# Optimization experiments

Hardware: AMD Instinct MI355X
Metric: run time of the kernel (lower is better)

Reference implementation:

```python
import jax, jax.numpy as jnp
import numpy as np

TOPK = 2
NUM_EXPERTS = 8

def setup_inputs() -> dict:
    key = jax.random.key(0)
    kx, kg, k1, k3, k2 = jax.random.split(key, 5)
    B, S, D, F, E = 1, 2048, 1024, 1024, NUM_EXPERTS
    x = jax.random.normal(kx, (B, S, D), dtype=jnp.float32)
    wg = jax.random.normal(kg, (E, D), dtype=jnp.float32) * (1.0 / np.sqrt(D))
    w1 = jax.random.normal(k1, (E, D, F), dtype=jnp.float32) * (1.0 / np.sqrt(D))
    w3 = jax.random.normal(k3, (E, D, F), dtype=jnp.float32) * (1.0 / np.sqrt(D))
    w2 = jax.random.normal(k2, (E, F, D), dtype=jnp.float32) * (1.0 / np.sqrt(F))
    return {"x": x, "wg": wg, "w1": w1, "w3": w3, "w2": w2}

def reference(x, wg, w1, w3, w2):
    # x: [B, S, D] -> tokens [N, D]
    D = x.shape[-1]
    E = wg.shape[0]
    xt = x.reshape(-1, D)
    # Gating: Linear(no bias) + softmax over experts
    logits = xt @ wg.T                      # [N, E]
    gates = jax.nn.softmax(logits, axis=-1)
    # Top-k selection, normalize weights (normalize_expert_weights=True),
    # routed_scaling_factor = 1.0
    weights, idx = jax.lax.top_k(gates, TOPK)      # [N, k]
    weights = weights / weights.sum(axis=-1, keepdims=True)
    # Per-token per-expert combine weight (dispatch+combine equivalent)
    comb = (jax.nn.one_hot(idx, E, dtype=xt.dtype) * weights[..., None]).sum(axis=1)  # [N, E]
    # SwiGLU experts (grouped GEMM equivalent, dense over experts)
    h = jnp.einsum('nd,edf->enf', xt, w1)   # gate proj
    u = jnp.einsum('nd,edf->enf', xt, w3)   # up proj
    a = jax.nn.silu(h) * u                  # [E, N, F]
    out = jnp.einsum('enf,efd,ne->nd', a, w2, comb)
    return out.reshape(x.shape), logits
```

## Files before the change

### kernel.cpp

```cpp
#include <hip/hip_runtime.h>
#include <stdint.h>

typedef unsigned short u16;
typedef __attribute__((ext_vector_type(8))) __bf16 bf16x8;
typedef __attribute__((ext_vector_type(4))) float f32x4;

#define MAXMT 40
#define N_TOK 2048
#define DDIM 1024
#define FDIM 1024

#define DEV static __device__ __forceinline__

DEV float bf2f(u16 u) {
    union { uint32_t i; float f; } v;
    v.i = ((uint32_t)u) << 16;
    return v.f;
}
DEV u16 f2bf(float f) {
    union { float f; uint32_t i; } v;
    v.f = f;
    uint32_t x = v.i;
    return (u16)((x + 0x7fffu + ((x >> 16) & 1u)) >> 16);
}

DEV void async_copy16(const u16* gsrc, u16* ldst) {
    __builtin_amdgcn_global_load_lds(
        (const __attribute__((address_space(1))) void*)(uintptr_t)gsrc,
        (__attribute__((address_space(3))) void*)(uint32_t)(uintptr_t)ldst,
        16, 0, 0);
}

DEV int sniff_fp(const void* p, int tid, int* scnt) {
    if (tid == 0) *scnt = 0;
    __syncthreads();
    u16 u = ((const u16*)p)[tid & 255];
    int e = (u >> 7) & 0xff;
    if (e != 0 && (e < 90 || e > 160)) atomicAdd(scnt, 1);
    __syncthreads();
    return *scnt > 64;
}

__global__ void k_mega(const void* __restrict__ x, const void* __restrict__ wg,
                       const void* __restrict__ w1, const void* __restrict__ w3,
                       const void* __restrict__ w2, u16* __restrict__ wt,
                       u16* __restrict__ xb, void* __restrict__ out_base,
                       int* __restrict__ te, float* __restrict__ tw) {
    __shared__ int scnt;
    __shared__ __align__(16) u16 sT[2][64 * 68];
    int z = blockIdx.z, tid = threadIdx.x;

    if (z >= 2) {
        int zz = z - 2;
        int mat = zz * 2 + (blockIdx.x >> 3);
        int which = mat >> 3, lm = mat & 7;
        const void* src0 = which == 0 ? w1 : (which == 1 ? w3 : w2);
        int fp = sniff_fp(src0, tid, &scnt);
        u16* dst = wt + (size_t)mat * 1048576;
        int rg = tid >> 4, cg = tid & 15;
        int r0 = blockIdx.y * 64, c0 = (blockIdx.x & 7) * 128;
        int rbase = r0 + rg * 4, cbase = c0 + cg * 4;

        u16 vA[4][4], vB[4][4];
        if (fp) {
            const float* sp = (const float*)src0 + (size_t)lm * 1048576;
            float4 fA[4], fB[4];
#pragma unroll
            for (int i = 0; i < 4; i++) fA[i] = *(const float4*)(sp + (size_t)(rbase + i) * 1024 + cbase);
#pragma unroll
            for (int i = 0; i < 4; i++) fB[i] = *(const float4*)(sp + (size_t)(rbase + i) * 1024 + cbase + 64);
#pragma unroll
            for (int i = 0; i < 4; i++) {
                vA[i][0] = f2bf(fA[i].x); vA[i][1] = f2bf(fA[i].y);
                vA[i][2] = f2bf(fA[i].z); vA[i][3] = f2bf(fA[i].w);
                vB[i][0] = f2bf(fB[i].x); vB[i][1] = f2bf(fB[i].y);
                vB[i][2] = f2bf(fB[i].z); vB[i][3] = f2bf(fB[i].w);
            }
        } else {
            const u16* sp = (const u16*)src0 + (size_t)lm * 1048576;
            uint2 uA[4], uB[4];
#pragma unroll
            for (int i = 0; i < 4; i++) uA[i] = *(const uint2*)(sp + (size_t)(rbase + i) * 1024 + cbase);
#pragma unroll
            for (int i = 0; i < 4; i++) uB[i] = *(const uint2*)(sp + (size_t)(rbase + i) * 1024 + cbase + 64);
#pragma unroll
            for (int i = 0; i < 4; i++) { *(uint2*)&vA[i][0] = uA[i]; *(uint2*)&vB[i][0] = uB[i]; }
        }
#pragma unroll
        for (int j = 0; j < 4; j++) {
            uint2 wa, wb;
            wa.x = (uint32_t)vA[0][j] | ((uint32_t)vA[1][j] << 16);
            wa.y = (uint32_t)vA[2][j] | ((uint32_t)vA[3][j] << 16);
            wb.x = (uint32_t)vB[0][j] | ((uint32_t)vB[1][j] << 16);
            wb.y = (uint32_t)vB[2][j] | ((uint32_t)vB[3][j] << 16);
            *(uint2*)&sT[0][(cg * 4 + j) * 68 + rg * 4] = wa;
            *(uint2*)&sT[1][(cg * 4 + j) * 68 + rg * 4] = wb;
        }
        __syncthreads();
        int cc = tid >> 2, seg = tid & 3;
#pragma unroll
        for (int b = 0; b < 2; b++) {
            const u16* spp = &sT[b][cc * 68 + seg * 16];
            uint2 q0 = *(const uint2*)(spp);
            uint2 q1 = *(const uint2*)(spp + 4);
            uint2 q2 = *(const uint2*)(spp + 8);
            uint2 q3 = *(const uint2*)(spp + 12);
            u16* dp = dst + (size_t)(c0 + b * 64 + cc) * 1024 + r0 + seg * 16;
            uint4 o0, o1;
            o0.x = q0.x; o0.y = q0.y; o0.z = q1.x; o0.w = q1.y;
            o1.x = q2.x; o1.y = q2.y; o1.z = q3.x; o1.w = q3.y;
            *(uint4*)dp = o0;
            *(uint4*)(dp + 8) = o1;
        }
    } else {
        int fp = sniff_fp(x, tid, &scnt);
        int gi = z * 256 + blockIdx.y * 16 + blockIdx.x;
        int wave = tid >> 6, lane = tid & 63;
        int n = gi * 4 + wave;
        float acc[8];
#pragma unroll
        for (int e = 0; e < 8; e++) acc[e] = 0.f;
        if (fp) {
            const float* xp = (const float*)x + (size_t)n * DDIM;
            const float* wp = (const float*)wg;
#pragma unroll
            for (int it = 0; it < 4; ++it) {
                int d = it * 256 + lane * 4;
                float4 xv = *(const float4*)(xp + d);
                u16 pk[4] = { f2bf(xv.x), f2bf(xv.y), f2bf(xv.z), f2bf(xv.w) };
                *(uint2*)&xb[(size_t)n * DDIM + d] = *(const uint2*)pk;
#pragma unroll
                for (int e = 0; e < 8; e++) {
                    float4 w4 = *(const float4*)(wp + e * DDIM + d);
                    acc[e] += xv.x * w4.x + xv.y * w4.y + xv.z * w4.z + xv.w * w4.w;
                }
            }
        } else {
            const u16* xp = (const u16*)x + (size_t)n * DDIM;
            const u16* wp = (const u16*)wg;
#pragma unroll
            for (int it = 0; it < 4; ++it) {
                int d = it * 256 + lane * 4;
                uint2 raw = *(const uint2*)(xp + d);
                *(uint2*)&xb[(size_t)n * DDIM + d] = raw;
                const u16* rp = (const u16*)&raw;
                float x0 = bf2f(rp[0]), x1 = bf2f(rp[1]), x2 = bf2f(rp[2]), x3 = bf2f(rp[3]);
#pragma unroll
                for (int e = 0; e < 8; e++) {
                    uint2 wr = *(const uint2*)(wp + e * DDIM + d);
                    const u16* wq = (const u16*)&wr;
                    acc[e] += x0 * bf2f(wq[0]) + x1 * bf2f(wq[1]) + x2 * bf2f(wq[2]) + x3 * bf2f(wq[3]);
                }
            }
        }
#pragma unroll
        for (int e = 0; e < 8; e++) {
            for (int off = 32; off; off >>= 1) acc[e] += __shfl_xor(acc[e], off);
        }
        if (lane < 8) {
            if (fp) ((float*)out_base + (size_t)N_TOK * DDIM)[n * 8 + lane] = acc[lane];
            else    ((u16*)out_base + (size_t)N_TOK * DDIM)[n * 8 + lane] = f2bf(acc[lane]);
        }
        if (lane == 0) {
            int e0 = 0; float b0 = acc[0];
            for (int e = 1; e < 8; e++) if (acc[e] > b0) { b0 = acc[e]; e0 = e; }
            int e1 = -1; float b1 = -1e30f;
            for (int e = 0; e < 8; e++) if (e != e0 && acc[e] > b1) { b1 = acc[e]; e1 = e; }
            float m = fmaxf(b0, b1);
            float x0 = __expf(b0 - m), x1 = __expf(b1 - m);
            float sden = x0 + x1;
            te[n * 2] = e0; te[n * 2 + 1] = e1;
            tw[n * 2] = x0 / sden; tw[n * 2 + 1] = x1 / sden;
        }
    }
}

__global__ void k_sched(const int* __restrict__ te, const float* __restrict__ tw,
                        int* __restrict__ pair_token, float* __restrict__ pair_weight,
                        int* __restrict__ ppos, int* __restrict__ sched) {
    __shared__ int cnt[8], cur[8];
    int t = threadIdx.x;
    if (t < 8) cnt[t] = 0;
    __syncthreads();
    for (int n = t; n < N_TOK; n += 256) {
        atomicAdd(&cnt[te[2 * n]], 1);
        atomicAdd(&cnt[te[2 * n + 1]], 1);
    }
    __syncthreads();
    if (t == 0) {
        int o = 0, mt = 0;
        for (int e = 0; e < 8; e++) {
            cur[e] = o;
            int c = cnt[e];
            for (int m0 = 0; m0 < c; m0 += 128) {
                sched[mt] = e;
                sched[MAXMT + mt] = o + m0;
                sched[2 * MAXMT + mt] = (c - m0 < 128) ? (c - m0) : 128;
                mt++;
            }
            o += c;
        }
        sched[3 * MAXMT] = mt;
        for (int i = mt; i < MAXMT; i++) { sched[i] = 0; sched[MAXMT + i] = 0; sched[2 * MAXMT + i] = 0; }
    }
    __syncthreads();
    for (int n = t; n < N_TOK; n += 256) {
#pragma unroll
        for (int s = 0; s < 2; s++) {
            int e = te[2 * n + s];
            int p = atomicAdd(&cur[e], 1);
            pair_token[p] = n;
            pair_weight[p] = tw[2 * n + s];
            ppos[2 * n + s] = p;
        }
    }
}

__launch_bounds__(256, 2)
__global__ void k_gemm13(const u16* __restrict__ xb, const u16* __restrict__ w1t,
                         const u16* __restrict__ w3t, const int* __restrict__ pair_token,
                         const int* __restrict__ sched, u16* __restrict__ Abuf) {
    __shared__ __align__(16) u16 smem[32768];

    int bn = blockIdx.x;
    int bm = blockIdx.y;
    int total = sched[3 * MAXMT];
    if (bm >= total) return;
    int e = sched[bm];
    int row0 = sched[MAXMT + bm];
    int rowsv = sched[2 * MAXMT + bm];

    int tid = threadIdx.x;
    int wave = tid >> 6, lane = tid & 63;
    int wm = wave & 1, wn = wave >> 1;
    int quad = lane >> 4, l15 = lane & 15;
    int lsub = lane >> 3, slot = lane & 7;

    const u16* gA[4]; int aoff[4];
#pragma unroll
    for (int c = 0; c < 4; c++) {
        int row = c * 32 + wave * 8 + lsub;
        int cr = row < rowsv ? row : 0;
        int tok = pair_token[row0 + cr];
        int gch = slot ^ (row & 7);
        gA[c] = xb + (size_t)tok * DDIM + gch * 8;
        aoff[c] = c * 2048 + wave * 512;
    }
    const u16* gB1[2]; const u16* gB3[2]; int b1off[2], b3off[2];
#pragma unroll
    for (int c = 0; c < 2; c++) {
        int row = c * 32 + wave * 8 + lsub;
        int gch = slot ^ (row & 7);
        int fcol = bn * 64 + row;
        gB1[c] = w1t + ((size_t)e * 1024 + fcol) * 1024 + gch * 8;
        gB3[c] = w3t + ((size_t)e * 1024 + fcol) * 1024 + gch * 8;
        b1off[c] = 8192 + c * 2048 + wave * 512;
        b3off[c] = 12288 + c * 2048 + wave * 512;
    }

    f32x4 acc_h[4][2], acc_u[4][2];
#pragma unroll
    for (int i = 0; i < 4; i++)
#pragma unroll
        for (int j = 0; j < 2; j++) { acc_h[i][j] = (f32x4)0.f; acc_u[i][j] = (f32x4)0.f; }

#pragma unroll
    for (int c = 0; c < 4; c++) async_copy16(gA[c], smem + aoff[c]);
#pragma unroll
    for (int c = 0; c < 2; c++) {
        async_copy16(gB1[c], smem + b1off[c]);
        async_copy16(gB3[c], smem + b3off[c]);
    }

    for (int kt = 0; kt < 16; ++kt) {
        int cur = kt & 1;
        u16* sbuf = smem + cur * 16384;
        __syncthreads();
        if (kt < 15) {
            int k1 = (kt + 1) * 64;
            u16* nbuf = smem + (cur ^ 1) * 16384;
#pragma unroll
            for (int c = 0; c < 4; c++) async_copy16(gA[c] + k1, nbuf + aoff[c]);
#pragma unroll
            for (int c = 0; c < 2; c++) {
                async_copy16(gB1[c] + k1, nbuf + b1off[c]);
                async_copy16(gB3[c] + k1, nbuf + b3off[c]);
            }
        }
        const u16* sA_  = sbuf;
        const u16* sB1_ = sbuf + 8192;
        const u16* sB3_ = sbuf + 12288;
#pragma unroll
        for (int kk = 0; kk < 2; ++kk) {
            bf16x8 a[4], b1[2], b3[2];
#pragma unroll
            for (int i = 0; i < 4; i++) {
                int m = wm * 64 + i * 16 + l15;
                int s = (kk * 4 + quad) ^ (m & 7);
                a[i] = *(const bf16x8*)&sA_[m * 64 + s * 8];
            }
#pragma unroll
            for (int j = 0; j < 2; j++) {
                int nn = wn * 32 + j * 16 + l15;
                int s = (kk * 4 + quad) ^ (nn & 7);
                b1[j] = *(const bf16x8*)&sB1_[nn * 64 + s * 8];
                b3[j] = *(const bf16x8*)&sB3_[nn * 64 + s * 8];
            }
#pragma unroll
            for (int i = 0; i < 4; i++)
#pragma unroll
                for (int j = 0; j < 2; j++) {
                    acc_h[i][j] = __builtin_amdgcn_mfma_f32_16x16x32_bf16(a[i], b1[j], acc_h[i][j], 0, 0, 0);
                    acc_u[i][j] = __builtin_amdgcn_mfma_f32_16x16x32_bf16(a[i], b3[j], acc_u[i][j], 0, 0, 0);
                }
        }
    }
    __syncthreads();
#pragma unroll
    for (int i = 0; i < 4; i++)
#pragma unroll
        for (int j = 0; j < 2; j++)
#pragma unroll
            for (int r = 0; r < 4; r++) {
                int row = wm * 64 + i * 16 + quad * 4 + r;
                int col = wn * 32 + j * 16 + l15;
                float h = acc_h[i][j][r], u = acc_u[i][j][r];
                smem[row * 72 + col] = f2bf(h * u / (1.0f + __expf(-h)));
            }
    __syncthreads();
    int rt = tid >> 1, half = tid & 1;
    if (rt < rowsv) {
        u16* dp = Abuf + (size_t)(row0 + rt) * FDIM + bn * 64 + half * 32;
        const u16* sp = &smem[rt * 72 + half * 32];
#pragma unroll
        for (int q = 0; q < 4; q++)
            *(uint4*)(dp + q * 8) = *(const uint4*)(sp + q * 8);
    }
}

__launch_bounds__(256, 3)
__global__ void k_gemm2(const u16* __restrict__ Abuf, const u16* __restrict__ w2t,
                        const int* __restrict__ sched, u16* __restrict__ Ybuf) {
    __shared__ __align__(16) u16 smem[24576];

    int bn = blockIdx.x;
    int bm = blockIdx.y;
    int total = sched[3 * MAXMT];
    if (bm >= total) return;
    int e = sched[bm];
    int row0 = sched[MAXMT + bm];
    int rowsv = sched[2 * MAXMT + bm];

    int tid = threadIdx.x;
    int wave = tid >> 6, lane = tid & 63;
    int wm = wave & 1, wn = wave >> 1;
    int quad = lane >> 4, l15 = lane & 15;
    int lsub = lane >> 3, slot = lane & 7;

    const u16* gA[4]; int aoff[4];
#pragma unroll
    for (int c = 0; c < 4; c++) {
        int row = c * 32 + wave * 8 + lsub;
        int cr = row < rowsv ? row : 0;
        int gch = slot ^ (row & 7);
        gA[c] = Abuf + (size_t)(row0 + cr) * FDIM + gch * 8;
        aoff[c] = c * 2048 + wave * 512;
    }
    const u16* gB[2]; int boff[2];
#pragma unroll
    for (int c = 0; c < 2; c++) {
        int row = c * 32 + wave * 8 + lsub;
        int gch = slot ^ (row & 7);
        int dcol = bn * 64 + row;
        gB[c] = w2t + ((size_t)e * 1024 + dcol) * 1024 + gch * 8;
        boff[c] = 8192 + c * 2048 + wave * 512;
    }

    f32x4 acc[4][2];
#pragma unroll
    for (int i = 0; i < 4; i++)
#pragma unroll
        for (int j = 0; j < 2; j++) acc[i][j] = (f32x4)0.f;

#pragma unroll
    for (int c = 0; c < 4; c++) async_copy16(gA[c], smem + aoff[c]);
#pragma unroll
    for (int c = 0; c < 2; c++) async_copy16(gB[c], smem + boff[c]);

    for (int kt = 0; kt < 16; ++kt) {
        int cur = kt & 1;
        u16* sbuf = smem + cur * 12288;
        __syncthreads();
        if (kt < 15) {
            int k1 = (kt + 1) * 64;
            u16* nbuf = smem + (cur ^ 1) * 12288;
#pragma unroll
            for (int c = 0; c < 4; c++) async_copy16(gA[c] + k1, nbuf + aoff[c]);
#pragma unroll
            for (int c = 0; c < 2; c++) async_copy16(gB[c] + k1, nbuf + boff[c]);
        }
        const u16* sA_ = sbuf;
        const u16* sB_ = sbuf + 8192;
#pragma unroll
        for (int kk = 0; kk < 2; ++kk) {
            bf16x8 a[4], b[2];
#pragma unroll
            for (int i = 0; i < 4; i++) {
                int m = wm * 64 + i * 16 + l15;
                int s = (kk * 4 + quad) ^ (m & 7);
                a[i] = *(const bf16x8*)&sA_[m * 64 + s * 8];
            }
#pragma unroll
            for (int j = 0; j < 2; j++) {
                int nn = wn * 32 + j * 16 + l15;
                int s = (kk * 4 + quad) ^ (nn & 7);
                b[j] = *(const bf16x8*)&sB_[nn * 64 + s * 8];
            }
#pragma unroll
            for (int i = 0; i < 4; i++)
#pragma unroll
                for (int j = 0; j < 2; j++)
                    acc[i][j] = __builtin_amdgcn_mfma_f32_16x16x32_bf16(a[i], b[j], acc[i][j], 0, 0, 0);
        }
    }
    __syncthreads();
#pragma unroll
    for (int i = 0; i < 4; i++)
#pragma unroll
        for (int j = 0; j < 2; j++)
#pragma unroll
            for (int r = 0; r < 4; r++) {
                int row = wm * 64 + i * 16 + quad * 4 + r;
                int col = wn * 32 + j * 16 + l15;
                smem[row * 72 + col] = f2bf(acc[i][j][r]);
            }
    __syncthreads();
    int rt = tid >> 1, half = tid & 1;
    if (rt < rowsv) {
        u16* dp = Ybuf + (size_t)(row0 + rt) * DDIM + bn * 64 + half * 32;
        const u16* sp = &smem[rt * 72 + half * 32];
#pragma unroll
        for (int q = 0; q < 4; q++)
            *(uint4*)(dp + q * 8) = *(const uint4*)(sp + q * 8);
    }
}

__global__ void k_combine(const u16* __restrict__ Y, const int* __restrict__ ppos,
                          const float* __restrict__ pwt, const void* __restrict__ x,
                          void* __restrict__ out) {
    __shared__ int scnt;
    int n = blockIdx.x, t = threadIdx.x;
    int fp = sniff_fp(x, t, &scnt);
    int p0 = ppos[2 * n], p1 = ppos[2 * n + 1];
    float w0 = pwt[p0], w1 = pwt[p1];
    uint2 a = *(const uint2*)(Y + (size_t)p0 * 1024 + t * 4);
    uint2 b = *(const uint2*)(Y + (size_t)p1 * 1024 + t * 4);
    const u16* ap = (const u16*)&a;
    const u16* bp = (const u16*)&b;
    float r[4];
#pragma unroll
    for (int j = 0; j < 4; j++) r[j] = w0 * bf2f(ap[j]) + w1 * bf2f(bp[j]);
    if (fp) {
        float4 o = { r[0], r[1], r[2], r[3] };
        *(float4*)((float*)out + (size_t)n * 1024 + t * 4) = o;
    } else {
        u16 o[4] = { f2bf(r[0]), f2bf(r[1]), f2bf(r[2]), f2bf(r[3]) };
        *(uint2*)((u16*)out + (size_t)n * 1024 + t * 4) = *(const uint2*)o;
    }
}

extern "C" void kernel_launch(void* const* d_in, const int* in_sizes, int n_in,
                              void* d_out, int out_size, void* d_ws, size_t ws_size,
                              hipStream_t stream) {
    const void* x  = d_in[0];
    const void* wg = d_in[1];
    const void* w1 = d_in[2];
    const void* w3 = d_in[3];
    const void* w2 = d_in[4];

    u16* wt   = (u16*)d_ws;
    u16* w1t  = wt;
    u16* w3t  = wt + (size_t)8 * 1048576;
    u16* w2t  = wt + (size_t)16 * 1048576;
    u16* Abuf = wt + (size_t)24 * 1048576;
    u16* Ybuf = Abuf + (size_t)4096 * 1024;
    u16* xb   = Ybuf + (size_t)4096 * 1024;
    int*   te   = (int*)(xb + (size_t)N_TOK * DDIM);
    float* tw   = (float*)(te + 2 * N_TOK);
    int*   ptok = (int*)(tw + 2 * N_TOK);
    float* pwt  = (float*)(ptok + 2 * N_TOK);
    int*   ppos = (int*)(pwt + 2 * N_TOK);
    int*   sched = ppos + 2 * N_TOK;

    k_mega<<<dim3(16, 16, 14), 256, 0, stream>>>(x, wg, w1, w3, w2, wt, xb, d_out, te, tw);
    k_sched<<<1, 256, 0, stream>>>(te, tw, ptok, pwt, ppos, sched);
    k_gemm13<<<dim3(16, MAXMT), 256, 0, stream>>>(xb, w1t, w3t, ptok, sched, Abuf);
    k_gemm2<<<dim3(16, MAXMT), 256, 0, stream>>>(Abuf, w2t, sched, Ybuf);
    k_combine<<<2048, 256, 0, stream>>>(Ybuf, ppos, pwt, x, d_out);
}
```

Measured before the change: 201.3 us.

## Process four transpose tiles per block with register double-buffered prefetch

Each weight-transpose block now handles four 64x128 tiles in sequence, prefetching the next tile's global loads into registers while the current tile is transposed through double-buffered LDS. The transpose grid shrinks from 12 to 3 z-slices. This aims to hide global load latency and amortize per-block setup such as the fp sniff, at the cost of fewer blocks, more registers and doubled shared memory.

Result: slower. 210.4 us (+4.5%).

```diff
diff --git a/kernel.cpp b/kernel.cpp
--- a/kernel.cpp
+++ b/kernel.cpp
@@ -47,70 +47,103 @@
                        u16* __restrict__ xb, void* __restrict__ out_base,
                        int* __restrict__ te, float* __restrict__ tw) {
     __shared__ int scnt;
-    __shared__ __align__(16) u16 sT[2][64 * 68];
+    __shared__ __align__(16) u16 sT[2][2][64 * 68];
     int z = blockIdx.z, tid = threadIdx.x;
 
     if (z >= 2) {
-        int zz = z - 2;
-        int mat = zz * 2 + (blockIdx.x >> 3);
+        int bl = (z - 2) * 256 + blockIdx.y * 16 + blockIdx.x;
+        int mat = bl >> 5;
         int which = mat >> 3, lm = mat & 7;
         const void* src0 = which == 0 ? w1 : (which == 1 ? w3 : w2);
         int fp = sniff_fp(src0, tid, &scnt);
         u16* dst = wt + (size_t)mat * 1048576;
+        const float* spf = (const float*)src0 + (size_t)lm * 1048576;
+        const u16*  spb = (const u16*)src0 + (size_t)lm * 1048576;
         int rg = tid >> 4, cg = tid & 15;
-        int r0 = blockIdx.y * 64, c0 = (blockIdx.x & 7) * 128;
-        int rbase = r0 + rg * 4, cbase = c0 + cg * 4;
-
-        u16 vA[4][4], vB[4][4];
+        int base = (bl & 31) * 4;
+        int r0 = (base >> 3) * 64;
+        int rbase = r0 + rg * 4;
+        int c0q[4];
+#pragma unroll
+        for (int q = 0; q < 4; q++) c0q[q] = ((base + q) & 7) * 128;
+
+        float4 lfA[2][4], lfB[2][4];
+
         if (fp) {
-            const float* sp = (const float*)src0 + (size_t)lm * 1048576;
-            float4 fA[4], fB[4];
-#pragma unroll
-            for (int i = 0; i < 4; i++) fA[i] = *(const float4*)(sp + (size_t)(rbase + i) * 1024 + cbase);
-#pragma unroll
-            for (int i = 0; i < 4; i++) fB[i] = *(const float4*)(sp + (size_t)(rbase + i) * 1024 + cbase + 64);
 #pragma unroll
             for (int i = 0; i < 4; i++) {
-                vA[i][0] = f2bf(fA[i].x); vA[i][1] = f2bf(fA[i].y);
-                vA[i][2] = f2bf(fA[i].z); vA[i][3] = f2bf(fA[i].w);
-                vB[i][0] = f2bf(fB[i].x); vB[i][1] = f2bf(fB[i].y);
-                vB[i][2] = f2bf(fB[i].z); vB[i][3] = f2bf(fB[i].w);
+                lfA[0][i] = *(const float4*)(spf + (size_t)(rbase + i) * 1024 + c0q[0] + cg * 4);
+                lfB[0][i] = *(const float4*)(spf + (size_t)(rbase + i) * 1024 + c0q[0] + cg * 4 + 64);
             }
         } else {
-            const u16* sp = (const u16*)src0 + (size_t)lm * 1048576;
-            uint2 uA[4], uB[4];
-#pragma unroll
-            for (int i = 0; i < 4; i++) uA[i] = *(const uint2*)(sp + (size_t)(rbase + i) * 1024 + cbase);
-#pragma unroll
-            for (int i = 0; i < 4; i++) uB[i] = *(const uint2*)(sp + (size_t)(rbase + i) * 1024 + cbase + 64);
-#pragma unroll
-            for (int i = 0; i < 4; i++) { *(uint2*)&vA[i][0] = uA[i]; *(uint2*)&vB[i][0] = uB[i]; }
-        }
-#pragma unroll
-        for (int j = 0; j < 4; j++) {
-            uint2 wa, wb;
-            wa.x = (uint32_t)vA[0][j] | ((uint32_t)vA[1][j] << 16);
-            wa.y = (uint32_t)vA[2][j] | ((uint32_t)vA[3][j] << 16);
-            wb.x = (uint32_t)vB[0][j] | ((uint32_t)vB[1][j] << 16);
-            wb.y = (uint32_t)vB[2][j] | ((uint32_t)vB[3][j] << 16);
-            *(uint2*)&sT[0][(cg * 4 + j) * 68 + rg * 4] = wa;
-            *(uint2*)&sT[1][(cg * 4 + j) * 68 + rg * 4] = wb;
-        }
-        __syncthreads();
-        int cc = tid >> 2, seg = tid & 3;
-#pragma unroll
-        for (int b = 0; b < 2; b++) {
-            const u16* spp = &sT[b][cc * 68 + seg * 16];
-            uint2 q0 = *(const uint2*)(spp);
-            uint2 q1 = *(const uint2*)(spp + 4);
-            uint2 q2 = *(const uint2*)(spp + 8);
-            uint2 q3 = *(const uint2*)(spp + 12);
-            u16* dp = dst + (size_t)(c0 + b * 64 + cc) * 1024 + r0 + seg * 16;
-            uint4 o0, o1;
-            o0.x = q0.x; o0.y = q0.y; o0.z = q1.x; o0.w = q1.y;
-            o1.x = q2.x; o1.y = q2.y; o1.z = q3.x; o1.w = q3.y;
-            *(uint4*)dp = o0;
-            *(uint4*)(dp + 8) = o1;
+#pragma unroll
+            for (int i = 0; i < 4; i++) {
+                *(uint2*)&lfA[0][i] = *(const uint2*)(spb + (size_t)(rbase + i) * 1024 + c0q[0] + cg * 4);
+                *(uint2*)&lfB[0][i] = *(const uint2*)(spb + (size_t)(rbase + i) * 1024 + c0q[0] + cg * 4 + 64);
+            }
+        }
+
+#pragma unroll
+        for (int q = 0; q < 4; q++) {
+            int s = q & 1;
+            u16 vA[4][4], vB[4][4];
+            if (fp) {
+#pragma unroll
+                for (int i = 0; i < 4; i++) {
+                    vA[i][0] = f2bf(lfA[s][i].x); vA[i][1] = f2bf(lfA[s][i].y);
+                    vA[i][2] = f2bf(lfA[s][i].z); vA[i][3] = f2bf(lfA[s][i].w);
+                    vB[i][0] = f2bf(lfB[s][i].x); vB[i][1] = f2bf(lfB[s][i].y);
+                    vB[i][2] = f2bf(lfB[s][i].z); vB[i][3] = f2bf(lfB[s][i].w);
+                }
+            } else {
+#pragma unroll
+                for (int i = 0; i < 4; i++) {
+                    *(uint2*)&vA[i][0] = *(const uint2*)&lfA[s][i];
+                    *(uint2*)&vB[i][0] = *(const uint2*)&lfB[s][i];
+                }
+            }
+#pragma unroll
+            for (int j = 0; j < 4; j++) {
+                uint2 wa, wb;
+                wa.x = (uint32_t)vA[0][j] | ((uint32_t)vA[1][j] << 16);
+                wa.y = (uint32_t)vA[2][j] | ((uint32_t)vA[3][j] << 16);
+                wb.x = (uint32_t)vB[0][j] | ((uint32_t)vB[1][j] << 16);
+                wb.y = (uint32_t)vB[2][j] | ((uint32_t)vB[3][j] << 16);
+                *(uint2*)&sT[s][0][(cg * 4 + j) * 68 + rg * 4] = wa;
+                *(uint2*)&sT[s][1][(cg * 4 + j) * 68 + rg * 4] = wb;
+            }
+            if (q < 3) {
+                int s2 = s ^ 1;
+                if (fp) {
+#pragma unroll
+                    for (int i = 0; i < 4; i++) {
+                        lfA[s2][i] = *(const float4*)(spf + (size_t)(rbase + i) * 1024 + c0q[q + 1] + cg * 4);
+                        lfB[s2][i] = *(const float4*)(spf + (size_t)(rbase + i) * 1024 + c0q[q + 1] + cg * 4 + 64);
+                    }
+                } else {
+#pragma unroll
+                    for (int i = 0; i < 4; i++) {
+                        *(uint2*)&lfA[s2][i] = *(const uint2*)(spb + (size_t)(rbase + i) * 1024 + c0q[q + 1] + cg * 4);
+                        *(uint2*)&lfB[s2][i] = *(const uint2*)(spb + (size_t)(rbase + i) * 1024 + c0q[q + 1] + cg * 4 + 64);
+                    }
+                }
+            }
+            __syncthreads();
+            int cc = tid >> 2, seg = tid & 3;
+#pragma unroll
+            for (int b = 0; b < 2; b++) {
+                const u16* spp = &sT[s][b][cc * 68 + seg * 16];
+                uint2 q0 = *(const uint2*)(spp);
+                uint2 q1 = *(const uint2*)(spp + 4);
+                uint2 q2 = *(const uint2*)(spp + 8);
+                uint2 q3 = *(const uint2*)(spp + 12);
+                u16* dp = dst + (size_t)(c0q[q] + b * 64 + cc) * 1024 + r0 + seg * 16;
+                uint4 o0, o1;
+                o0.x = q0.x; o0.y = q0.y; o0.z = q1.x; o0.w = q1.y;
+                o1.x = q2.x; o1.y = q2.y; o1.z = q3.x; o1.w = q3.y;
+                *(uint4*)dp = o0;
+                *(uint4*)(dp + 8) = o1;
+            }
         }
     } else {
         int fp = sniff_fp(x, tid, &scnt);
@@ -492,7 +525,7 @@
     int*   ppos = (int*)(pwt + 2 * N_TOK);
     int*   sched = ppos + 2 * N_TOK;
 
-    k_mega<<<dim3(16, 16, 14), 256, 0, stream>>>(x, wg, w1, w3, w2, wt, xb, d_out, te, tw);
+    k_mega<<<dim3(16, 16, 5), 256, 0, stream>>>(x, wg, w1, w3, w2, wt, xb, d_out, te, tw);
     k_sched<<<1, 256, 0, stream>>>(te, tw, ptok, pwt, ppos, sched);
     k_gemm13<<<dim3(16, MAXMT), 256, 0, stream>>>(xb, w1t, w3t, ptok, sched, Abuf);
     k_gemm2<<<dim3(16, MAXMT), 256, 0, stream>>>(Abuf, w2t, sched, Ybuf);
```

## Move w2 transpose into the scheduling kernel to overlap with routing

Applied to the files above, without the earlier changes.

The w2 weight transpose/convert moves out of the first mega kernel into a new kernel that also runs the single-block routing schedule. The schedule step no longer runs alone as a one-block launch but alongside the w2 transpose blocks, which shortens the first kernel. The cost is an extra grid of mostly idle blocks in z=4, and the w2 work now runs after gating instead of alongside it.

Result: slower. 206.4 us (+2.5%).

```diff
diff --git a/kernel.cpp b/kernel.cpp
--- a/kernel.cpp
+++ b/kernel.cpp
@@ -41,10 +41,106 @@
     return *scnt > 64;
 }
 
+DEV void transpose_tile(const void* src0, int lm, int fp, u16* dst,
+                        int r0, int c0, int tid, u16 (*sT)[64 * 68]) {
+    int rg = tid >> 4, cg = tid & 15;
+    int rbase = r0 + rg * 4, cbase = c0 + cg * 4;
+
+    u16 vA[4][4], vB[4][4];
+    if (fp) {
+        const float* sp = (const float*)src0 + (size_t)lm * 1048576;
+        float4 fA[4], fB[4];
+#pragma unroll
+        for (int i = 0; i < 4; i++) fA[i] = *(const float4*)(sp + (size_t)(rbase + i) * 1024 + cbase);
+#pragma unroll
+        for (int i = 0; i < 4; i++) fB[i] = *(const float4*)(sp + (size_t)(rbase + i) * 1024 + cbase + 64);
+#pragma unroll
+        for (int i = 0; i < 4; i++) {
+            vA[i][0] = f2bf(fA[i].x); vA[i][1] = f2bf(fA[i].y);
+            vA[i][2] = f2bf(fA[i].z); vA[i][3] = f2bf(fA[i].w);
+            vB[i][0] = f2bf(fB[i].x); vB[i][1] = f2bf(fB[i].y);
+            vB[i][2] = f2bf(fB[i].z); vB[i][3] = f2bf(fB[i].w);
+        }
+    } else {
+        const u16* sp = (const u16*)src0 + (size_t)lm * 1048576;
+        uint2 uA[4], uB[4];
+#pragma unroll
+        for (int i = 0; i < 4; i++) uA[i] = *(const uint2*)(sp + (size_t)(rbase + i) * 1024 + cbase);
+#pragma unroll
+        for (int i = 0; i < 4; i++) uB[i] = *(const uint2*)(sp + (size_t)(rbase + i) * 1024 + cbase + 64);
+#pragma unroll
+        for (int i = 0; i < 4; i++) { *(uint2*)&vA[i][0] = uA[i]; *(uint2*)&vB[i][0] = uB[i]; }
+    }
+#pragma unroll
+    for (int j = 0; j < 4; j++) {
+        uint2 wa, wb;
+        wa.x = (uint32_t)vA[0][j] | ((uint32_t)vA[1][j] << 16);
+        wa.y = (uint32_t)vA[2][j] | ((uint32_t)vA[3][j] << 16);
+        wb.x = (uint32_t)vB[0][j] | ((uint32_t)vB[1][j] << 16);
+        wb.y = (uint32_t)vB[2][j] | ((uint32_t)vB[3][j] << 16);
+        *(uint2*)&sT[0][(cg * 4 + j) * 68 + rg * 4] = wa;
+        *(uint2*)&sT[1][(cg * 4 + j) * 68 + rg * 4] = wb;
+    }
+    __syncthreads();
+    int cc = tid >> 2, seg = tid & 3;
+#pragma unroll
+    for (int b = 0; b < 2; b++) {
+        const u16* spp = &sT[b][cc * 68 + seg * 16];
+        uint2 q0 = *(const uint2*)(spp);
+        uint2 q1 = *(const uint2*)(spp + 4);
+        uint2 q2 = *(const uint2*)(spp + 8);
+        uint2 q3 = *(const uint2*)(spp + 12);
+        u16* dp = dst + (size_t)(c0 + b * 64 + cc) * 1024 + r0 + seg * 16;
+        uint4 o0, o1;
+        o0.x = q0.x; o0.y = q0.y; o0.z = q1.x; o0.w = q1.y;
+        o1.x = q2.x; o1.y = q2.y; o1.z = q3.x; o1.w = q3.y;
+        *(uint4*)dp = o0;
+        *(uint4*)(dp + 8) = o1;
+    }
+}
+
+DEV void run_sched(const int* te, const float* tw, int* pair_token, float* pair_weight,
+                   int* ppos, int* sched, int t, int* cnt, int* cur) {
+    if (t < 8) cnt[t] = 0;
+    __syncthreads();
+    for (int n = t; n < N_TOK; n += 256) {
+        atomicAdd(&cnt[te[2 * n]], 1);
+        atomicAdd(&cnt[te[2 * n + 1]], 1);
+    }
+    __syncthreads();
+    if (t == 0) {
+        int o = 0, mt = 0;
+        for (int e = 0; e < 8; e++) {
+            cur[e] = o;
+            int c = cnt[e];
+            for (int m0 = 0; m0 < c; m0 += 128) {
+                sched[mt] = e;
+                sched[MAXMT + mt] = o + m0;
+                sched[2 * MAXMT + mt] = (c - m0 < 128) ? (c - m0) : 128;
+                mt++;
+            }
+            o += c;
+        }
+        sched[3 * MAXMT] = mt;
+        for (int i = mt; i < MAXMT; i++) { sched[i] = 0; sched[MAXMT + i] = 0; sched[2 * MAXMT + i] = 0; }
+    }
+    __syncthreads();
+    for (int n = t; n < N_TOK; n += 256) {
+#pragma unroll
+        for (int s = 0; s < 2; s++) {
+            int e = te[2 * n + s];
+            int p = atomicAdd(&cur[e], 1);
+            pair_token[p] = n;
+            pair_weight[p] = tw[2 * n + s];
+            ppos[2 * n + s] = p;
+        }
+    }
+}
+
 __global__ void k_mega(const void* __restrict__ x, const void* __restrict__ wg,
                        const void* __restrict__ w1, const void* __restrict__ w3,
-                       const void* __restrict__ w2, u16* __restrict__ wt,
-                       u16* __restrict__ xb, void* __restrict__ out_base,
+                       u16* __restrict__ wt, u16* __restrict__ xb,
+                       void* __restrict__ out_base,
                        int* __restrict__ te, float* __restrict__ tw) {
     __shared__ int scnt;
     __shared__ __align__(16) u16 sT[2][64 * 68];
@@ -53,65 +149,10 @@
     if (z >= 2) {
         int zz = z - 2;
         int mat = zz * 2 + (blockIdx.x >> 3);
-        int which = mat >> 3, lm = mat & 7;
-        const void* src0 = which == 0 ? w1 : (which == 1 ? w3 : w2);
+        const void* src0 = (mat >> 3) == 0 ? w1 : w3;
         int fp = sniff_fp(src0, tid, &scnt);
-        u16* dst = wt + (size_t)mat * 1048576;
-        int rg = tid >> 4, cg = tid & 15;
-        int r0 = blockIdx.y * 64, c0 = (blockIdx.x & 7) * 128;
-        int rbase = r0 + rg * 4, cbase = c0 + cg * 4;
-
-        u16 vA[4][4], vB[4][4];
-        if (fp) {
-            const float* sp = (const float*)src0 + (size_t)lm * 1048576;
-            float4 fA[4], fB[4];
-#pragma unroll
-            for (int i = 0; i < 4; i++) fA[i] = *(const float4*)(sp + (size_t)(rbase + i) * 1024 + cbase);
-#pragma unroll
-            for (int i = 0; i < 4; i++) fB[i] = *(const float4*)(sp + (size_t)(rbase + i) * 1024 + cbase + 64);
-#pragma unroll
-            for (int i = 0; i < 4; i++) {
-                vA[i][0] = f2bf(fA[i].x); vA[i][1] = f2bf(fA[i].y);
-                vA[i][2] = f2bf(fA[i].z); vA[i][3] = f2bf(fA[i].w);
-                vB[i][0] = f2bf(fB[i].x); vB[i][1] = f2bf(fB[i].y);
-                vB[i][2] = f2bf(fB[i].z); vB[i][3] = f2bf(fB[i].w);
-            }
-        } else {
-            const u16* sp = (const u16*)src0 + (size_t)lm * 1048576;
-            uint2 uA[4], uB[4];
-#pragma unroll
-            for (int i = 0; i < 4; i++) uA[i] = *(const uint2*)(sp + (size_t)(rbase + i) * 1024 + cbase);
-#pragma unroll
-            for (int i = 0; i < 4; i++) uB[i] = *(const uint2*)(sp + (size_t)(rbase + i) * 1024 + cbase + 64);
-#pragma unroll
-            for (int i = 0; i < 4; i++) { *(uint2*)&vA[i][0] = uA[i]; *(uint2*)&vB[i][0] = uB[i]; }
-        }
-#pragma unroll
-        for (int j = 0; j < 4; j++) {
-            uint2 wa, wb;
-            wa.x = (uint32_t)vA[0][j] | ((uint32_t)vA[1][j] << 16);
-            wa.y = (uint32_t)vA[2][j] | ((uint32_t)vA[3][j] << 16);
-            wb.x = (uint32_t)vB[0][j] | ((uint32_t)vB[1][j] << 16);
-            wb.y = (uint32_t)vB[2][j] | ((uint32_t)vB[3][j] << 16);
-            *(uint2*)&sT[0][(cg * 4 + j) * 68 + rg * 4] = wa;
-            *(uint2*)&sT[1][(cg * 4 + j) * 68 + rg * 4] = wb;
-        }
-        __syncthreads();
-        int cc = tid >> 2, seg = tid & 3;
-#pragma unroll
-        for (int b = 0; b < 2; b++) {
-            const u16* spp = &sT[b][cc * 68 + seg * 16];
-            uint2 q0 = *(const uint2*)(spp);
-            uint2 q1 = *(const uint2*)(spp + 4);
-            uint2 q2 = *(const uint2*)(spp + 8);
-            uint2 q3 = *(const uint2*)(spp + 12);
-            u16* dp = dst + (size_t)(c0 + b * 64 + cc) * 1024 + r0 + seg * 16;
-            uint4 o0, o1;
-            o0.x = q0.x; o0.y = q0.y; o0.z = q1.x; o0.w = q1.y;
-            o1.x = q2.x; o1.y = q2.y; o1.z = q3.x; o1.w = q3.y;
-            *(uint4*)dp = o0;
-            *(uint4*)(dp + 8) = o1;
-        }
+        transpose_tile(src0, mat & 7, fp, wt + (size_t)mat * 1048576,
+                       blockIdx.y * 64, (blockIdx.x & 7) * 128, tid, sT);
     } else {
         int fp = sniff_fp(x, tid, &scnt);
         int gi = z * 256 + blockIdx.y * 16 + blockIdx.x;
@@ -175,44 +216,23 @@
     }
 }
 
-__global__ void k_sched(const int* __restrict__ te, const float* __restrict__ tw,
-                        int* __restrict__ pair_token, float* __restrict__ pair_weight,
+__global__ void k_trw2s(const void* __restrict__ w2, u16* __restrict__ wt,
+                        const int* __restrict__ te, const float* __restrict__ tw,
+                        int* __restrict__ ptok, float* __restrict__ pwt,
                         int* __restrict__ ppos, int* __restrict__ sched) {
-    __shared__ int cnt[8], cur[8];
-    int t = threadIdx.x;
-    if (t < 8) cnt[t] = 0;
-    __syncthreads();
-    for (int n = t; n < N_TOK; n += 256) {
-        atomicAdd(&cnt[te[2 * n]], 1);
-        atomicAdd(&cnt[te[2 * n + 1]], 1);
-    }
-    __syncthreads();
-    if (t == 0) {
-        int o = 0, mt = 0;
-        for (int e = 0; e < 8; e++) {
-            cur[e] = o;
-            int c = cnt[e];
-            for (int m0 = 0; m0 < c; m0 += 128) {
-                sched[mt] = e;
-                sched[MAXMT + mt] = o + m0;
-                sched[2 * MAXMT + mt] = (c - m0 < 128) ? (c - m0) : 128;
-                mt++;
-            }
-            o += c;
-        }
-        sched[3 * MAXMT] = mt;
-        for (int i = mt; i < MAXMT; i++) { sched[i] = 0; sched[MAXMT + i] = 0; sched[2 * MAXMT + i] = 0; }
-    }
-    __syncthreads();
-    for (int n = t; n < N_TOK; n += 256) {
-#pragma unroll
-        for (int s = 0; s < 2; s++) {
-            int e = te[2 * n + s];
-            int p = atomicAdd(&cur[e], 1);
-            pair_token[p] = n;
-            pair_weight[p] = tw[2 * n + s];
-            ppos[2 * n + s] = p;
-        }
+    __shared__ int scnt;
+    __shared__ __align__(16) u16 sT[2][64 * 68];
+    __shared__ int cnt8[8], cur8[8];
+    int z = blockIdx.z, tid = threadIdx.x;
+
+    if (z < 4) {
+        int mat = 16 + z * 2 + (blockIdx.x >> 3);
+        int fp = sniff_fp(w2, tid, &scnt);
+        transpose_tile(w2, mat & 7, fp, wt + (size_t)mat * 1048576,
+                       blockIdx.y * 64, (blockIdx.x & 7) * 128, tid, sT);
+    } else {
+        if (blockIdx.x == 0 && blockIdx.y == 0)
+            run_sched(te, tw, ptok, pwt, ppos, sched, tid, cnt8, cur8);
     }
 }
 
@@ -492,8 +512,8 @@
     int*   ppos = (int*)(pwt + 2 * N_TOK);
     int*   sched = ppos + 2 * N_TOK;
 
-    k_mega<<<dim3(16, 16, 14), 256, 0, stream>>>(x, wg, w1, w3, w2, wt, xb, d_out, te, tw);
-    k_sched<<<1, 256, 0, stream>>>(te, tw, ptok, pwt, ppos, sched);
+    k_mega<<<dim3(16, 16, 10), 256, 0, stream>>>(x, wg, w1, w3, wt, xb, d_out, te, tw);
+    k_trw2s<<<dim3(16, 16, 5), 256, 0, stream>>>(w2, wt, te, tw, ptok, pwt, ppos, sched);
     k_gemm13<<<dim3(16, MAXMT), 256, 0, stream>>>(xb, w1t, w3t, ptok, sched, Abuf);
     k_gemm2<<<dim3(16, MAXMT), 256, 0, stream>>>(Abuf, w2t, sched, Ybuf);
     k_combine<<<2048, 256, 0, stream>>>(Ybuf, ppos, pwt, x, d_out);
```

## Fuse w1/w3 fp32-to-bf16 transpose into gate/up GEMM B-tile staging

Applied to the files above, without the earlier changes.

Removes the separate pre-pass that converted and transposed w1 and w3 into a bf16 workspace. The gate/up GEMM now reads the original weights directly through registers, converts them with a packed bf16 conversion instruction, and writes them transposed into a swizzled shared-memory tile, prefetching two k-steps ahead. This cuts the global write and re-read of 16 weight matrices and shrinks the prep launch. The cost is that each of the roughly 16×40 GEMM blocks re-converts its weight slice, the global loads now go through registers instead of asynchronous copies to LDS, and each block does extra fp32 weight reads.

New measurement: 226.1 us. 12.3% more time.

```diff
diff --git a/kernel.cpp b/kernel.cpp
--- a/kernel.cpp
+++ b/kernel.cpp
@@ -23,6 +23,11 @@
     uint32_t x = v.i;
     return (u16)((x + 0x7fffu + ((x >> 16) & 1u)) >> 16);
 }
+DEV uint32_t pkbf(float a, float b) {
+    uint32_t r;
+    asm("v_cvt_pk_bf16_f32 %0, %1, %2" : "=v"(r) : "v"(a), "v"(b));
+    return r;
+}
 
 DEV void async_copy16(const u16* gsrc, u16* ldst) {
     __builtin_amdgcn_global_load_lds(
@@ -41,8 +46,65 @@
     return *scnt > 64;
 }
 
+DEV void transpose_tile(const void* src0, int lm, int fp, u16* dst,
+                        int r0, int c0, int tid, u16 (*sT)[64 * 68]) {
+    int rg = tid >> 4, cg = tid & 15;
+    int rbase = r0 + rg * 4, cbase = c0 + cg * 4;
+
+    u16 vA[4][4], vB[4][4];
+    if (fp) {
+        const float* sp = (const float*)src0 + (size_t)lm * 1048576;
+        float4 fA[4], fB[4];
+#pragma unroll
+        for (int i = 0; i < 4; i++) fA[i] = *(const float4*)(sp + (size_t)(rbase + i) * 1024 + cbase);
+#pragma unroll
+        for (int i = 0; i < 4; i++) fB[i] = *(const float4*)(sp + (size_t)(rbase + i) * 1024 + cbase + 64);
+#pragma unroll
+        for (int i = 0; i < 4; i++) {
+            vA[i][0] = f2bf(fA[i].x); vA[i][1] = f2bf(fA[i].y);
+            vA[i][2] = f2bf(fA[i].z); vA[i][3] = f2bf(fA[i].w);
+            vB[i][0] = f2bf(fB[i].x); vB[i][1] = f2bf(fB[i].y);
+            vB[i][2] = f2bf(fB[i].z); vB[i][3] = f2bf(fB[i].w);
+        }
+    } else {
+        const u16* sp = (const u16*)src0 + (size_t)lm * 1048576;
+        uint2 uA[4], uB[4];
+#pragma unroll
+        for (int i = 0; i < 4; i++) uA[i] = *(const uint2*)(sp + (size_t)(rbase + i) * 1024 + cbase);
+#pragma unroll
+        for (int i = 0; i < 4; i++) uB[i] = *(const uint2*)(sp + (size_t)(rbase + i) * 1024 + cbase + 64);
+#pragma unroll
+        for (int i = 0; i < 4; i++) { *(uint2*)&vA[i][0] = uA[i]; *(uint2*)&vB[i][0] = uB[i]; }
+    }
+#pragma unroll
+    for (int j = 0; j < 4; j++) {
+        uint2 wa, wb;
+        wa.x = (uint32_t)vA[0][j] | ((uint32_t)vA[1][j] << 16);
+        wa.y = (uint32_t)vA[2][j] | ((uint32_t)vA[3][j] << 16);
+        wb.x = (uint32_t)vB[0][j] | ((uint32_t)vB[1][j] << 16);
+        wb.y = (uint32_t)vB[2][j] | ((uint32_t)vB[3][j] << 16);
+        *(uint2*)&sT[0][(cg * 4 + j) * 68 + rg * 4] = wa;
+        *(uint2*)&sT[1][(cg * 4 + j) * 68 + rg * 4] = wb;
+    }
+    __syncthreads();
+    int cc = tid >> 2, seg = tid & 3;
+#pragma unroll
+    for (int b = 0; b < 2; b++) {
+        const u16* spp = &sT[b][cc * 68 + seg * 16];
+        uint2 q0 = *(const uint2*)(spp);
+        uint2 q1 = *(const uint2*)(spp + 4);
+        uint2 q2 = *(const uint2*)(spp + 8);
+        uint2 q3 = *(const uint2*)(spp + 12);
+        u16* dp = dst + (size_t)(c0 + b * 64 + cc) * 1024 + r0 + seg * 16;
+        uint4 o0, o1;
+        o0.x = q0.x; o0.y = q0.y; o0.z = q1.x; o0.w = q1.y;
+        o1.x = q2.x; o1.y = q2.y; o1.z = q3.x; o1.w = q3.y;
+        *(uint4*)dp = o0;
+        *(uint4*)(dp + 8) = o1;
+    }
+}
+
 __global__ void k_mega(const void* __restrict__ x, const void* __restrict__ wg,
-                       const void* __restrict__ w1, const void* __restrict__ w3,
                        const void* __restrict__ w2, u16* __restrict__ wt,
                        u16* __restrict__ xb, void* __restrict__ out_base,
                        int* __restrict__ te, float* __restrict__ tw) {
@@ -51,67 +113,10 @@
     int z = blockIdx.z, tid = threadIdx.x;
 
     if (z >= 2) {
-        int zz = z - 2;
-        int mat = zz * 2 + (blockIdx.x >> 3);
-        int which = mat >> 3, lm = mat & 7;
-        const void* src0 = which == 0 ? w1 : (which == 1 ? w3 : w2);
-        int fp = sniff_fp(src0, tid, &scnt);
-        u16* dst = wt + (size_t)mat * 1048576;
-        int rg = tid >> 4, cg = tid & 15;
-        int r0 = blockIdx.y * 64, c0 = (blockIdx.x & 7) * 128;
-        int rbase = r0 + rg * 4, cbase = c0 + cg * 4;
-
-        u16 vA[4][4], vB[4][4];
-        if (fp) {
-            const float* sp = (const float*)src0 + (size_t)lm * 1048576;
-            float4 fA[4], fB[4];
-#pragma unroll
-            for (int i = 0; i < 4; i++) fA[i] = *(const float4*)(sp + (size_t)(rbase + i) * 1024 + cbase);
-#pragma unroll
-            for (int i = 0; i < 4; i++) fB[i] = *(const float4*)(sp + (size_t)(rbase + i) * 1024 + cbase + 64);
-#pragma unroll
-            for (int i = 0; i < 4; i++) {
-                vA[i][0] = f2bf(fA[i].x); vA[i][1] = f2bf(fA[i].y);
-                vA[i][2] = f2bf(fA[i].z); vA[i][3] = f2bf(fA[i].w);
-                vB[i][0] = f2bf(fB[i].x); vB[i][1] = f2bf(fB[i].y);
-                vB[i][2] = f2bf(fB[i].z); vB[i][3] = f2bf(fB[i].w);
-            }
-        } else {
-            const u16* sp = (const u16*)src0 + (size_t)lm * 1048576;
-            uint2 uA[4], uB[4];
-#pragma unroll
-            for (int i = 0; i < 4; i++) uA[i] = *(const uint2*)(sp + (size_t)(rbase + i) * 1024 + cbase);
-#pragma unroll
-            for (int i = 0; i < 4; i++) uB[i] = *(const uint2*)(sp + (size_t)(rbase + i) * 1024 + cbase + 64);
-#pragma unroll
-            for (int i = 0; i < 4; i++) { *(uint2*)&vA[i][0] = uA[i]; *(uint2*)&vB[i][0] = uB[i]; }
-        }
-#pragma unroll
-        for (int j = 0; j < 4; j++) {
-            uint2 wa, wb;
-            wa.x = (uint32_t)vA[0][j] | ((uint32_t)vA[1][j] << 16);
-            wa.y = (uint32_t)vA[2][j] | ((uint32_t)vA[3][j] << 16);
-            wb.x = (uint32_t)vB[0][j] | ((uint32_t)vB[1][j] << 16);
-            wb.y = (uint32_t)vB[2][j] | ((uint32_t)vB[3][j] << 16);
-            *(uint2*)&sT[0][(cg * 4 + j) * 68 + rg * 4] = wa;
-            *(uint2*)&sT[1][(cg * 4 + j) * 68 + rg * 4] = wb;
-        }
-        __syncthreads();
-        int cc = tid >> 2, seg = tid & 3;
-#pragma unroll
-        for (int b = 0; b < 2; b++) {
-            const u16* spp = &sT[b][cc * 68 + seg * 16];
-            uint2 q0 = *(const uint2*)(spp);
-            uint2 q1 = *(const uint2*)(spp + 4);
-            uint2 q2 = *(const uint2*)(spp + 8);
-            uint2 q3 = *(const uint2*)(spp + 12);
-            u16* dp = dst + (size_t)(c0 + b * 64 + cc) * 1024 + r0 + seg * 16;
-            uint4 o0, o1;
-            o0.x = q0.x; o0.y = q0.y; o0.z = q1.x; o0.w = q1.y;
-            o1.x = q2.x; o1.y = q2.y; o1.z = q3.x; o1.w = q3.y;
-            *(uint4*)dp = o0;
-            *(uint4*)(dp + 8) = o1;
-        }
+        int mat = 16 + (z - 2) * 2 + (blockIdx.x >> 3);
+        int fp = sniff_fp(w2, tid, &scnt);
+        transpose_tile(w2, mat & 7, fp, wt + (size_t)mat * 1048576,
+                       blockIdx.y * 64, (blockIdx.x & 7) * 128, tid, sT);
     } else {
         int fp = sniff_fp(x, tid, &scnt);
         int gi = z * 256 + blockIdx.y * 16 + blockIdx.x;
@@ -216,11 +221,46 @@
     }
 }
 
+DEV void bstage_load(const void* w, int fp, size_t matoff, int krow0, int fcol0,
+                     int rg, int cg, float4 r[4]) {
+    if (fp) {
+        const float* sp = (const float*)w + matoff + (size_t)(krow0 + rg * 4) * 1024 + fcol0 + cg * 4;
+#pragma unroll
+        for (int i = 0; i < 4; i++) r[i] = *(const float4*)(sp + i * 1024);
+    } else {
+        const u16* sp = (const u16*)w + matoff + (size_t)(krow0 + rg * 4) * 1024 + fcol0 + cg * 4;
+#pragma unroll
+        for (int i = 0; i < 4; i++) *(uint2*)&r[i] = *(const uint2*)(sp + i * 1024);
+    }
+}
+DEV void bstage_write(u16* sB, const float4 r[4], int fp, int rg, int cg) {
+#pragma unroll
+    for (int j = 0; j < 4; j++) {
+        int n = cg * 4 + j;
+        uint2 w;
+        if (fp) {
+            w.x = pkbf(reinterpret_cast<const float*>(&r[0])[j], reinterpret_cast<const float*>(&r[1])[j]);
+            w.y = pkbf(reinterpret_cast<const float*>(&r[2])[j], reinterpret_cast<const float*>(&r[3])[j]);
+        } else {
+            const u16* e0 = reinterpret_cast<const u16*>(&r[0]);
+            const u16* e1 = reinterpret_cast<const u16*>(&r[1]);
+            const u16* e2 = reinterpret_cast<const u16*>(&r[2]);
+            const u16* e3 = reinterpret_cast<const u16*>(&r[3]);
+            w.x = (uint32_t)e0[j] | ((uint32_t)e1[j] << 16);
+            w.y = (uint32_t)e2[j] | ((uint32_t)e3[j] << 16);
+        }
+        *(uint2*)&sB[n * 64 + ((rg ^ (n & 14)) << 2)] = w;
+    }
+}
+
 __launch_bounds__(256, 2)
-__global__ void k_gemm13(const u16* __restrict__ xb, const u16* __restrict__ w1t,
-                         const u16* __restrict__ w3t, const int* __restrict__ pair_token,
+__global__ void k_gemm13(const u16* __restrict__ xb, const void* __restrict__ w1,
+                         const void* __restrict__ w3, const int* __restrict__ pair_token,
                          const int* __restrict__ sched, u16* __restrict__ Abuf) {
+    __shared__ int scnt;
     __shared__ __align__(16) u16 smem[32768];
+
+    int fp = sniff_fp(w1, threadIdx.x, &scnt);
 
     int bn = blockIdx.x;
     int bm = blockIdx.y;
@@ -235,6 +275,7 @@
     int wm = wave & 1, wn = wave >> 1;
     int quad = lane >> 4, l15 = lane & 15;
     int lsub = lane >> 3, slot = lane & 7;
+    int rg = tid >> 4, cg = tid & 15;
 
     const u16* gA[4]; int aoff[4];
 #pragma unroll
@@ -246,17 +287,10 @@
         gA[c] = xb + (size_t)tok * DDIM + gch * 8;
         aoff[c] = c * 2048 + wave * 512;
     }
-    const u16* gB1[2]; const u16* gB3[2]; int b1off[2], b3off[2];
-#pragma unroll
-    for (int c = 0; c < 2; c++) {
-        int row = c * 32 + wave * 8 + lsub;
-        int gch = slot ^ (row & 7);
-        int fcol = bn * 64 + row;
-        gB1[c] = w1t + ((size_t)e * 1024 + fcol) * 1024 + gch * 8;
-        gB3[c] = w3t + ((size_t)e * 1024 + fcol) * 1024 + gch * 8;
-        b1off[c] = 8192 + c * 2048 + wave * 512;
-        b3off[c] = 12288 + c * 2048 + wave * 512;
-    }
+
+    size_t moff = (size_t)e * 1048576;
+    int fcol0 = bn * 64;
+    float4 rB1[4], rB3[4];
 
     f32x4 acc_h[4][2], acc_u[4][2];
 #pragma unroll
@@ -264,32 +298,28 @@
 #pragma unroll
         for (int j = 0; j < 2; j++) { acc_h[i][j] = (f32x4)0.f; acc_u[i][j] = (f32x4)0.f; }
 
+    bstage_load(w1, fp, moff, 0, fcol0, rg, cg, rB1);
+    bstage_load(w3, fp, moff, 0, fcol0, rg, cg, rB3);
+    bstage_write(smem + 8192, rB1, fp, rg, cg);
+    bstage_write(smem + 12288, rB3, fp, rg, cg);
 #pragma unroll
     for (int c = 0; c < 4; c++) async_copy16(gA[c], smem + aoff[c]);
-#pragma unroll
-    for (int c = 0; c < 2; c++) {
-        async_copy16(gB1[c], smem + b1off[c]);
-        async_copy16(gB3[c], smem + b3off[c]);
-    }
+    bstage_load(w1, fp, moff, 64, fcol0, rg, cg, rB1);
+    bstage_load(w3, fp, moff, 64, fcol0, rg, cg, rB3);
 
     for (int kt = 0; kt < 16; ++kt) {
         int cur = kt & 1;
-        u16* sbuf = smem + cur * 16384;
+        u16* bufC = smem + cur * 16384;
+        u16* bufN = smem + (cur ^ 1) * 16384;
         __syncthreads();
         if (kt < 15) {
             int k1 = (kt + 1) * 64;
-            u16* nbuf = smem + (cur ^ 1) * 16384;
-#pragma unroll
-            for (int c = 0; c < 4; c++) async_copy16(gA[c] + k1, nbuf + aoff[c]);
-#pragma unroll
-            for (int c = 0; c < 2; c++) {
-                async_copy16(gB1[c] + k1, nbuf + b1off[c]);
-                async_copy16(gB3[c] + k1, nbuf + b3off[c]);
-            }
-        }
-        const u16* sA_  = sbuf;
-        const u16* sB1_ = sbuf + 8192;
-        const u16* sB3_ = sbuf + 12288;
+#pragma unroll
+            for (int c = 0; c < 4; c++) async_copy16(gA[c] + k1, bufN + aoff[c]);
+        }
+        const u16* sA_  = bufC;
+        const u16* sB1_ = bufC + 8192;
+        const u16* sB3_ = bufC + 12288;
 #pragma unroll
         for (int kk = 0; kk < 2; ++kk) {
             bf16x8 a[4], b1[2], b3[2];
@@ -302,7 +332,7 @@
 #pragma unroll
             for (int j = 0; j < 2; j++) {
                 int nn = wn * 32 + j * 16 + l15;
-                int s = (kk * 4 + quad) ^ (nn & 7);
+                int s = (kk * 4 + quad) ^ ((nn >> 1) & 7);
                 b1[j] = *(const bf16x8*)&sB1_[nn * 64 + s * 8];
                 b3[j] = *(const bf16x8*)&sB3_[nn * 64 + s * 8];
             }
@@ -313,6 +343,15 @@
                     acc_h[i][j] = __builtin_amdgcn_mfma_f32_16x16x32_bf16(a[i], b1[j], acc_h[i][j], 0, 0, 0);
                     acc_u[i][j] = __builtin_amdgcn_mfma_f32_16x16x32_bf16(a[i], b3[j], acc_u[i][j], 0, 0, 0);
                 }
+        }
+        if (kt < 15) {
+            bstage_write(bufN + 8192, rB1, fp, rg, cg);
+            bstage_write(bufN + 12288, rB3, fp, rg, cg);
+            if (kt < 14) {
+                int k2 = (kt + 2) * 64;
+                bstage_load(w1, fp, moff, k2, fcol0, rg, cg, rB1);
+                bstage_load(w3, fp, moff, k2, fcol0, rg, cg, rB3);
+            }
         }
     }
     __syncthreads();
@@ -479,8 +518,6 @@
     const void* w2 = d_in[4];
 
     u16* wt   = (u16*)d_ws;
-    u16* w1t  = wt;
-    u16* w3t  = wt + (size_t)8 * 1048576;
     u16* w2t  = wt + (size_t)16 * 1048576;
     u16* Abuf = wt + (size_t)24 * 1048576;
     u16* Ybuf = Abuf + (size_t)4096 * 1024;
@@ -492,9 +529,9 @@
     int*   ppos = (int*)(pwt + 2 * N_TOK);
     int*   sched = ppos + 2 * N_TOK;
 
-    k_mega<<<dim3(16, 16, 14), 256, 0, stream>>>(x, wg, w1, w3, w2, wt, xb, d_out, te, tw);
+    k_mega<<<dim3(16, 16, 6), 256, 0, stream>>>(x, wg, w2, wt, xb, d_out, te, tw);
     k_sched<<<1, 256, 0, stream>>>(te, tw, ptok, pwt, ppos, sched);
-    k_gemm13<<<dim3(16, MAXMT), 256, 0, stream>>>(xb, w1t, w3t, ptok, sched, Abuf);
+    k_gemm13<<<dim3(16, MAXMT), 256, 0, stream>>>(xb, w1, w3, ptok, sched, Abuf);
     k_gemm2<<<dim3(16, MAXMT), 256, 0, stream>>>(Abuf, w2t, sched, Ybuf);
     k_combine<<<2048, 256, 0, stream>>>(Ybuf, ppos, pwt, x, d_out);
 }
```
